# Performance work log

Measured on AMD Instinct MI355X. Metric: run time of the kernel, lower is better.

## Reference

```python
import math
import jax, jax.numpy as jnp
import numpy as np
from jax import lax

RADIUS = 3
KSIZE = 2 * RADIUS + 1  # 7
TOP_K = 8
SINKHORN_ITERS = 5


def _box_sum(x, h_axis, w_axis):
    # sum pooling with same padding over spatial axes
    wd = [1] * x.ndim
    wd[h_axis] = KSIZE
    wd[w_axis] = KSIZE
    pads = [(0, 0)] * x.ndim
    pads[h_axis] = (RADIUS, RADIUS)
    pads[w_axis] = (RADIUS, RADIUS)
    return lax.reduce_window(x, 0.0, lax.add, tuple(wd), (1,) * x.ndim, pads)


def geo_validate(src_pos, cand_pos, H, W):
    # src_pos [B,N,2], cand_pos [B,N,K,2] -> score [B,N,K]
    B, N, K, _ = cand_pos.shape
    src = src_pos.reshape(B, H, W, 1, 2)
    cand = cand_pos.reshape(B, H, W, K, 2)
    disp = cand - src  # [B,H,W,K,2]
    # count_include_pad=False -> divide by number of valid (in-bounds) taps
    cnt = _box_sum(jnp.ones((1, H, W, 1, 1), disp.dtype), 1, 2)
    mean = _box_sum(disp, 1, 2) / cnt
    mean_sq = _box_sum(disp * disp, 1, 2) / cnt
    var = jnp.clip(mean_sq - mean * mean, 0.0)
    total_var = var.sum(-1).reshape(B, N, K)
    return 1.0 / (1.0 + 100.0 * total_var)


def optimal_transport(scores, dustbin):
    B, M, N = scores.shape
    row = jnp.broadcast_to(dustbin, (B, M, 1))
    col = jnp.broadcast_to(dustbin, (B, 1, N))
    corner = jnp.zeros((B, 1, 1), scores.dtype)
    Z = jnp.concatenate([jnp.concatenate([scores, row], 2),
                         jnp.concatenate([col, corner], 2)], 1)  # [B,M+1,N+1]
    norm = -math.log(M + N)
    log_mu = jnp.full((M + 1,), norm, scores.dtype).at[M].set(math.log(N) + norm)
    log_nu = jnp.full((N + 1,), norm, scores.dtype).at[N].set(math.log(M) + norm)
    log_mu = jnp.broadcast_to(log_mu, (B, M + 1))
    log_nu = jnp.broadcast_to(log_nu, (B, N + 1))

    def body(_, uv):
        u, v = uv
        u = log_mu - jax.nn.logsumexp(Z + v[:, None, :], axis=2)
        v = log_nu - jax.nn.logsumexp(Z + u[:, :, None], axis=1)
        return (u, v)

    u0 = jnp.zeros((B, M + 1), scores.dtype)
    v0 = jnp.zeros((B, N + 1), scores.dtype)
    u, v = lax.fori_loop(0, SINKHORN_ITERS, body, (u0, v0))
    log_assign = Z + u[:, :, None] + v[:, None, :]
    return log_assign[:, :M, :N]


def solve_weighted_affine(src_pts, dst_pts, weights):
    # src/dst [B,N,2], weights [B,N,1] -> H_mat [B,3,3]
    B, N, _ = src_pts.shape
    w = weights[..., 0]
    w = w / jnp.clip(w.sum(1, keepdims=True), 1e-6)
    x, y = src_pts[..., 0], src_pts[..., 1]
    one = jnp.ones_like(x)
    zero = jnp.zeros_like(x)
    row_x = jnp.stack([x, y, one, zero, zero, zero], -1)   # [B,N,6]
    row_y = jnp.stack([zero, zero, zero, x, y, one], -1)
    A = jnp.concatenate([row_x, row_y], 1)                 # [B,2N,6]
    b = jnp.concatenate([dst_pts[..., 0], dst_pts[..., 1]], 1)[..., None]
    wd = jnp.concatenate([w, w], 1)[..., None]             # [B,2N,1]
    Aw = A * wd
    AtWA = jnp.einsum('bni,bnj->bij', Aw, A) + 1e-4 * jnp.eye(6, dtype=A.dtype)
    AtWb = jnp.einsum('bni,bnk->bik', Aw, b)
    p = jnp.linalg.solve(AtWA, AtWb)[..., 0]               # [B,6]
    a_, b_, c_, d_, e_, f_ = [p[:, i] for i in range(6)]
    z = jnp.zeros_like(a_)
    o = jnp.ones_like(a_)
    return jnp.stack([a_, b_, c_, d_, e_, f_, z, z, o], -1).reshape(B, 3, 3)


def matcher_forward(feat_A, feat_B, pos_A, pos_B, dustbin_score, geo_weight,
                    current_temp, H, W):
    B, N, C = feat_A.shape
    temp = current_temp[0]
    nA = feat_A / jnp.clip(jnp.linalg.norm(feat_A, axis=-1, keepdims=True), 1e-12)
    nB = feat_B / jnp.clip(jnp.linalg.norm(feat_B, axis=-1, keepdims=True), 1e-12)
    scores = jnp.einsum('bnc,bmc->bnm', nA, nB) / temp      # [B,N,N]
    log_assign = optimal_transport(scores, dustbin_score[0])
    ot_prob = jnp.exp(log_assign)
    topk_vals, topk_idx = lax.top_k(ot_prob, TOP_K)          # [B,N,K]
    bidx = jnp.arange(B)[:, None, None]
    topk_pos = pos_B[bidx, topk_idx]                         # [B,N,K,2]
    geo = geo_validate(pos_A, topk_pos, H, W)                # [B,N,K]
    gw = jnp.clip(geo_weight[0], 0.0, 2.0)
    combined = topk_vals + gw * geo
    soft = jax.nn.softmax(combined / temp, axis=-1)
    refined_warp = (topk_pos * soft[..., None]).sum(2)       # [B,N,2]
    conf = (soft * topk_vals).sum(-1, keepdims=True)         # [B,N,1]
    H_mat = solve_weighted_affine(pos_A, refined_warp, conf)
    return refined_warp, conf, H_mat


def setup_inputs() -> dict:
    key = jax.random.key(0)
    kA, kB, kP = jax.random.split(key, 3)
    B, H, W, C = 2, 64, 64, 128
    N = H * W
    feat_A = jax.random.normal(kA, (B, N, C), jnp.float32)
    feat_B = jax.random.normal(kB, (B, N, C), jnp.float32)
    # dense grid positions, normalized to [0,1]
    ys, xs = jnp.meshgrid(jnp.arange(H, dtype=jnp.float32),
                          jnp.arange(W, dtype=jnp.float32), indexing='ij')
    grid = jnp.stack([xs, ys], -1).reshape(1, N, 2) / float(max(H, W))
    pos_A = jnp.broadcast_to(grid, (B, N, 2))
    pos_B = pos_A + 0.01 * jax.random.normal(kP, (B, N, 2), jnp.float32)
    return {
        'feat_A': feat_A, 'feat_B': feat_B,
        'pos_A': pos_A, 'pos_B': pos_B,
        'dustbin_score': jnp.full((1,), -1.0, jnp.float32),
        'geo_weight': jnp.full((1,), 0.5, jnp.float32),
        'current_temp': jnp.full((1,), 0.1, jnp.float32),
        'H': H, 'W': W,
    }


def reference(feat_A, feat_B, pos_A, pos_B, dustbin_score, geo_weight,
              current_temp, H, W):
    return matcher_forward(feat_A, feat_B, pos_A, pos_B, dustbin_score,
                           geo_weight, current_temp, H, W)
```

## Files before the change

kernel.cpp:

```cpp
#include <hip/hip_runtime.h>
#include <math.h>

#define UVS 4104

#define OFF_ZU    33554432ul
#define OFF_WV    (OFF_ZU + 2*UVS)
#define OFF_RN    (OFF_WV + 2*UVS)
#define OFF_PARTS (OFF_RN + 16384)
#define OFF_TKV   (OFF_PARTS + 4194304)
#define OFF_TKP   (OFF_TKV + 65536)
#define OFF_DP    (OFF_TKP + 131072)
#define OFF_GEO   (OFF_DP + 131072)
#define OFF_SUM   (OFF_GEO + 65536)

#define EXPC    0.0001220703125f
#define HALFC   0.5f

#define PLANE   1048576

typedef __attribute__((ext_vector_type(8))) short bf16x8;
typedef __attribute__((ext_vector_type(4))) float f32x4;

static __device__ __forceinline__ unsigned f2bf(float x) {
    unsigned u = __float_as_uint(x);
    return (u + 0x7FFFu + ((u >> 16) & 1u)) >> 16;
}
static __device__ __forceinline__ float bf2f(unsigned h) { return __uint_as_float(h << 16); }

__global__ __launch_bounds__(256) void init_kernel(float* __restrict__ wv)
{
    int i = blockIdx.x * 256 + threadIdx.x;
    if (i < 2 * UVS) wv[i] = 1.0f;
}

__global__ __launch_bounds__(256) void norms_kernel(
    const float* __restrict__ fA, const float* __restrict__ fB, float* __restrict__ rn)
{
    int t = threadIdx.x;
    int rowg = blockIdx.x * 4 + (t >> 6);
    int lane = t & 63;
    const float* f = (rowg < 8192) ? fA : fB;
    int r = rowg & 8191;
    float x0 = f[(size_t)r * 128 + lane];
    float x1 = f[(size_t)r * 128 + 64 + lane];
    float s = x0 * x0 + x1 * x1;
    #pragma unroll
    for (int off = 32; off > 0; off >>= 1) s += __shfl_xor(s, off, 64);
    if (lane == 0) rn[rowg] = 1.f / fmaxf(sqrtf(s), 1e-12f);
}

__global__ __launch_bounds__(256) void pack_kernel(
    const float* __restrict__ fA, const float* __restrict__ fB, short* __restrict__ pk)
{
    int gt = blockIdx.x * 256 + threadIdx.x;
    int tensor = gt >> 17;
    int t = gt & 131071;
    int fr = t & 15;
    int kc = (t >> 4) & 15;
    int rb = (t >> 8) & 255;
    int b  = t >> 16;
    const float* src = tensor ? fB : fA;
    const float* p = src + ((size_t)(b * 4096 + rb * 16 + fr)) * 128 + kc * 8;
    float4 v0 = *(const float4*)p;
    float4 v1 = *(const float4*)(p + 4);
    float el[8] = {v0.x, v0.y, v0.z, v0.w, v1.x, v1.y, v1.z, v1.w};
    unsigned h[8], l[8];
    #pragma unroll
    for (int e = 0; e < 8; e++) { h[e] = f2bf(el[e]); l[e] = f2bf(el[e] - bf2f(h[e])); }
    uint4 hw = make_uint4(h[0] | (h[1] << 16), h[2] | (h[3] << 16),
                          h[4] | (h[5] << 16), h[6] | (h[7] << 16));
    uint4 lw = make_uint4(l[0] | (l[1] << 16), l[2] | (l[3] << 16),
                          l[4] | (l[5] << 16), l[6] | (l[7] << 16));
    size_t off = ((size_t)(b * 256 + rb)) * 2048 + kc * 128 + fr * 8;
    short* hi = pk + (size_t)tensor * 2 * PLANE;
    *(uint4*)(hi + off) = hw;
    *(uint4*)(hi + PLANE + off) = lw;
}

__global__ __launch_bounds__(256) void gemm_mfma(
    const short* __restrict__ pk, const float* __restrict__ rn,
    const float* __restrict__ temp, float* __restrict__ E0)
{
    __shared__ short Bs[16384];
    int b = blockIdx.z;
    int i0 = blockIdx.y * 64, j0 = blockIdx.x * 64;
    int t = threadIdx.x;
    int wave = t >> 6, lane = t & 63;
    int fr = lane & 15;
    int quad = lane >> 4;

    const short* gBhi = pk + 2 * (size_t)PLANE + ((size_t)(b * 256 + (j0 >> 4))) * 2048;
    const short* gBlo = gBhi + PLANE;
    #pragma unroll
    for (int c = 0; c < 4; c++) {
        int ch = c * 256 + t;
        *(uint4*)&Bs[ch * 8]        = *(const uint4*)(gBhi + ch * 8);
        *(uint4*)&Bs[8192 + ch * 8] = *(const uint4*)(gBlo + ch * 8);
    }

    const short* Abase_hi = pk + ((size_t)(b * 256 + (i0 >> 4) + wave)) * 2048;
    const short* Abase_lo = Abase_hi + PLANE;
    bf16x8 ah[4], al[4];
    #pragma unroll
    for (int s = 0; s < 4; s++) {
        ah[s] = *(const bf16x8*)(Abase_hi + s * 512 + lane * 8);
        al[s] = *(const bf16x8*)(Abase_lo + s * 512 + lane * 8);
    }
    __syncthreads();

    f32x4 acc[4] = {f32x4{0,0,0,0}, f32x4{0,0,0,0}, f32x4{0,0,0,0}, f32x4{0,0,0,0}};
    #pragma unroll
    for (int s = 0; s < 4; s++) {
        int lo = s * 512 + lane * 8;
        #pragma unroll
        for (int nb = 0; nb < 4; nb++) {
            bf16x8 bh = *(const bf16x8*)&Bs[nb * 2048 + lo];
            bf16x8 bl = *(const bf16x8*)&Bs[8192 + nb * 2048 + lo];
            acc[nb] = __builtin_amdgcn_mfma_f32_16x16x32_bf16(ah[s], bh, acc[nb], 0, 0, 0);
            acc[nb] = __builtin_amdgcn_mfma_f32_16x16x32_bf16(al[s], bh, acc[nb], 0, 0, 0);
            acc[nb] = __builtin_amdgcn_mfma_f32_16x16x32_bf16(ah[s], bl, acc[nb], 0, 0, 0);
        }
    }

    float invt = 1.f / temp[0];
    int m0 = i0 + wave * 16 + quad * 4;
    float ra[4];
    #pragma unroll
    for (int rr = 0; rr < 4; rr++) ra[rr] = rn[b * 4096 + m0 + rr] * invt;
    #pragma unroll
    for (int nb = 0; nb < 4; nb++) {
        int col = j0 + nb * 16 + fr;
        float rbv = rn[8192 + b * 4096 + col];
        #pragma unroll
        for (int rr = 0; rr < 4; rr++)
            E0[((size_t)(b * 4096 + m0 + rr)) * 4096 + col] = __expf(acc[nb][rr] * (ra[rr] * rbv));
    }
}

__global__ __launch_bounds__(64) void sink_fused(
    const float* __restrict__ E0, float* __restrict__ zu, const float* __restrict__ wv,
    const float* __restrict__ dbp, float* __restrict__ parts)
{
    int b = blockIdx.z;
    int lane = threadIdx.x;
    int ch = blockIdx.x;
    const float* wb = wv + b * UVS;
    float edb = __expf(dbp[0]);

    if (ch == 0) {
        float sv = 0.f;
        #pragma unroll
        for (int c = 0; c < 16; c++) {
            f32x4 w4 = *(const f32x4*)(wb + lane * 4 + c * 256);
            sv += (w4.x + w4.y) + (w4.z + w4.w);
        }
        #pragma unroll
        for (int off = 32; off > 0; off >>= 1) sv += __shfl_xor(sv, off, 64);
        if (lane == 0) zu[b * UVS + 4096] = HALFC / (edb * sv + wb[4096]);
    }

    float dtail = edb * wb[4096];
    f32x4 cacc[16];
    #pragma unroll
    for (int c = 0; c < 16; c++) cacc[c] = f32x4{0, 0, 0, 0};

    const float* Eb = E0 + ((size_t)b << 24);
    int base = lane * 4;

    for (int r = 0; r < 8; r++) {
        int row = ch * 8 + r;
        const float* Erow = Eb + ((size_t)row << 12);
        f32x4 x4[16];
        #pragma unroll
        for (int c = 0; c < 16; c++) x4[c] = *(const f32x4*)(Erow + base + c * 256);
        f32x4 rs4 = f32x4{0, 0, 0, 0};
        #pragma unroll
        for (int c = 0; c < 16; c++) {
            f32x4 w4 = *(const f32x4*)(wb + base + c * 256);
            rs4 += x4[c] * w4;
        }
        float rs = (rs4.x + rs4.y) + (rs4.z + rs4.w);
        #pragma unroll
        for (int off = 32; off > 0; off >>= 1) rs += __shfl_xor(rs, off, 64);
        float zi = EXPC / (rs + dtail);
        if (lane == 0) zu[b * UVS + row] = zi;
        #pragma unroll
        for (int c = 0; c < 16; c++) cacc[c] += x4[c] * zi;
    }

    float* pp = parts + ((size_t)(b * 512 + ch)) * 4096;
    #pragma unroll
    for (int c = 0; c < 16; c++) *(f32x4*)(pp + base + c * 256) = cacc[c];
}

__global__ __launch_bounds__(256) void sink_vB(
    const float* __restrict__ parts, const float* __restrict__ zu,
    float* __restrict__ wv, const float* __restrict__ dbp)
{
    int b = blockIdx.z;
    int t = threadIdx.x;
    float edb = __expf(dbp[0]);
    if (blockIdx.x < 16) {
        int j = blockIdx.x * 256 + t;
        float s = 0.f;
        #pragma unroll 16
        for (int ch = 0; ch < 512; ch++) s += parts[((size_t)(b * 512 + ch)) * 4096 + j];
        float total = s + edb * zu[b * UVS + 4096];
        wv[b * UVS + j] = EXPC / total;
    } else {
        __shared__ float red[256];
        float s = 0.f;
        for (int i = t; i < 4096; i += 256) s += zu[b * UVS + i];
        red[t] = s; __syncthreads();
        for (int off = 128; off > 0; off >>= 1) {
            if (t < off) red[t] += red[t + off];
            __syncthreads();
        }
        if (t == 0)
            wv[b * UVS + 4096] = HALFC / (edb * red[0] + zu[b * UVS + 4096]);
    }
}

#define FCMPSWAP(a, b) { float _mx = fmaxf(a, b), _mn = fminf(a, b); (a) = _mx; (b) = _mn; }
__global__ __launch_bounds__(256) void topk_kernel(
    const float* __restrict__ E0, const float* __restrict__ zu, const float* __restrict__ wv,
    const float* __restrict__ posA, const float* __restrict__ posB,
    float* __restrict__ tkv, float* __restrict__ tkp, float* __restrict__ dp)
{
    int wave = threadIdx.x >> 6;
    int lane = threadIdx.x & 63;
    int row = blockIdx.x * 4 + wave;
    int b = row >> 12; int i = row & 4095;
    const float* Erow = E0 + (size_t)row * 4096;
    const float* wb = wv + b * UVS;

    __shared__ unsigned long long cand[4][64];
    __shared__ int ccnt[4];
    if (lane == 0) ccnt[wave] = 0;

    f32x4 q[16];
    float s[8] = {0, 0, 0, 0, 0, 0, 0, 0};
    #pragma unroll
    for (int c = 0; c < 16; c++) {
        int j = c * 256 + lane * 4;
        f32x4 x = *(const f32x4*)(Erow + j);
        f32x4 w = *(const f32x4*)(wb + j);
        q[c] = x * w;
        float el[4] = {q[c].x, q[c].y, q[c].z, q[c].w};
        #pragma unroll
        for (int e = 0; e < 4; e++) {
            float xv = el[e];
            s[7] = __builtin_amdgcn_fmed3f(s[6], s[7], xv);
            s[6] = __builtin_amdgcn_fmed3f(s[5], s[6], xv);
            s[5] = __builtin_amdgcn_fmed3f(s[4], s[5], xv);
            s[4] = __builtin_amdgcn_fmed3f(s[3], s[4], xv);
            s[3] = __builtin_amdgcn_fmed3f(s[2], s[3], xv);
            s[2] = __builtin_amdgcn_fmed3f(s[1], s[2], xv);
            s[1] = __builtin_amdgcn_fmed3f(s[0], s[1], xv);
            s[0] = fmaxf(s[0], xv);
        }
    }

    #pragma unroll
    for (int st = 0; st < 6; st++) {
        int off = 1 << st;
        float o[8];
        #pragma unroll
        for (int r = 0; r < 8; r++) o[r] = __shfl_xor(s[r], off, 64);
        float m[8];
        #pragma unroll
        for (int r = 0; r < 8; r++) m[r] = fmaxf(s[r], o[7 - r]);
        FCMPSWAP(m[0], m[4]); FCMPSWAP(m[1], m[5]); FCMPSWAP(m[2], m[6]); FCMPSWAP(m[3], m[7]);
        FCMPSWAP(m[0], m[2]); FCMPSWAP(m[1], m[3]); FCMPSWAP(m[4], m[6]); FCMPSWAP(m[5], m[7]);
        FCMPSWAP(m[0], m[1]); FCMPSWAP(m[2], m[3]); FCMPSWAP(m[4], m[5]); FCMPSWAP(m[6], m[7]);
        #pragma unroll
        for (int r = 0; r < 8; r++) s[r] = m[r];
    }
    float t8 = s[7];

    __syncthreads();

    #pragma unroll
    for (int c = 0; c < 16; c++) {
        float el[4] = {q[c].x, q[c].y, q[c].z, q[c].w};
        #pragma unroll
        for (int e = 0; e < 4; e++) {
            if (el[e] >= t8) {
                int j = c * 256 + lane * 4 + e;
                unsigned long long key =
                    ((unsigned long long)__float_as_uint(el[e]) << 32) | (unsigned)(4095 - j);
                int slot = atomicAdd(&ccnt[wave], 1);
                if (slot < 64) cand[wave][slot] = key;
            }
        }
    }
    __syncthreads();

    int cnt = ccnt[wave]; if (cnt > 64) cnt = 64;
    if (lane < cnt) {
        unsigned long long my = cand[wave][lane];
        int rank = 0;
        for (int j2 = 0; j2 < cnt; j2++) rank += (cand[wave][j2] > my) ? 1 : 0;
        if (rank < 8) {
            int idx = 4095 - (int)(my & 0xFFFFFFFFu);
            float candv = __uint_as_float((unsigned)(my >> 32));
            float val = candv * zu[b * UVS + i];
            float px = posB[((size_t)(b * 4096 + idx)) * 2 + 0];
            float py = posB[((size_t)(b * 4096 + idx)) * 2 + 1];
            float ax = posA[((size_t)(b * 4096 + i)) * 2 + 0];
            float ay = posA[((size_t)(b * 4096 + i)) * 2 + 1];
            size_t base = ((size_t)(b * 4096 + i)) * 8 + rank;
            tkv[base] = val;
            tkp[base * 2 + 0] = px; tkp[base * 2 + 1] = py;
            dp[((size_t)((b * 8 + rank) * 2 + 0)) * 4096 + i] = px - ax;
            dp[((size_t)((b * 8 + rank) * 2 + 1)) * 4096 + i] = py - ay;
        }
    }
}

__global__ __launch_bounds__(256) void geo_kernel(
    const float* __restrict__ dp, float* __restrict__ geo)
{
    int tid = blockIdx.x * 256 + threadIdx.x;
    int n = tid & 4095; int bk = tid >> 12;
    int b = bk >> 3; int k = bk & 7;
    int h = n >> 6, w = n & 63;
    const float* dpx = dp + ((size_t)(bk * 2 + 0)) * 4096;
    const float* dpy = dp + ((size_t)(bk * 2 + 1)) * 4096;
    float sx = 0, sy = 0, sxx = 0, syy = 0, cnt = 0;
    #pragma unroll
    for (int dy = -3; dy <= 3; dy++) {
        int hh = h + dy; if ((unsigned)hh >= 64u) continue;
        #pragma unroll
        for (int dx = -3; dx <= 3; dx++) {
            int ww = w + dx; if ((unsigned)ww >= 64u) continue;
            int nn = (hh << 6) + ww;
            float vx = dpx[nn], vy = dpy[nn];
            sx += vx; sy += vy; sxx += vx * vx; syy += vy * vy; cnt += 1.f;
        }
    }
    float inv = 1.f / cnt;
    float mx = sx * inv, my = sy * inv;
    float varx = fmaxf(sxx * inv - mx * mx, 0.f);
    float vary = fmaxf(syy * inv - my * my, 0.f);
    geo[((size_t)(b * 4096 + n)) * 8 + k] = 1.f / (1.f + 100.f * (varx + vary));
}

__global__ __launch_bounds__(256) void refine_kernel(
    const float* __restrict__ tkv, const float* __restrict__ geo,
    const float* __restrict__ tkp, const float* __restrict__ gwp,
    const float* __restrict__ tpp, float* __restrict__ out)
{
    int tid = blockIdx.x * 256 + threadIdx.x;
    float gw = fminf(fmaxf(gwp[0], 0.f), 2.f);
    float invt = 1.f / tpp[0];
    size_t base = (size_t)tid * 8;
    float cb[8], vv[8];
    float mx = -INFINITY;
    #pragma unroll
    for (int k = 0; k < 8; k++) { vv[k] = tkv[base + k]; cb[k] = vv[k] + gw * geo[base + k]; mx = fmaxf(mx, cb[k]); }
    float e[8], se = 0;
    #pragma unroll
    for (int k = 0; k < 8; k++) { e[k] = __expf((cb[k] - mx) * invt); se += e[k]; }
    float wx = 0, wy = 0, cf = 0; float inv = 1.f / se;
    #pragma unroll
    for (int k = 0; k < 8; k++) {
        float s = e[k] * inv;
        wx += s * tkp[(base + k) * 2 + 0];
        wy += s * tkp[(base + k) * 2 + 1];
        cf += s * vv[k];
    }
    out[(size_t)tid * 2 + 0] = wx;
    out[(size_t)tid * 2 + 1] = wy;
    out[16384 + tid] = cf;
}

__global__ __launch_bounds__(256) void affine_reduce(
    const float* __restrict__ posA, const float* __restrict__ out, double* __restrict__ sums)
{
    int b = blockIdx.x; int t = threadIdx.x;
    double acc[12] = {0,0,0,0,0,0,0,0,0,0,0,0};
    for (int n = t; n < 4096; n += 256) {
        size_t idx = (size_t)b * 4096 + n;
        float x = posA[idx * 2], y = posA[idx * 2 + 1];
        float dx = out[idx * 2], dy = out[idx * 2 + 1];
        float c = out[16384 + idx];
        double cd = (double)c;
        double cx = cd * x, cy = cd * y;
        acc[0] += cx * x;  acc[1] += cx * y;  acc[2] += cy * y;
        acc[3] += cx;      acc[4] += cy;      acc[5] += cd;
        acc[6] += cx * dx; acc[7] += cy * dx; acc[8] += cd * dx;
        acc[9] += cx * dy; acc[10] += cy * dy; acc[11] += cd * dy;
    }
    __shared__ double red[256];
    for (int s = 0; s < 12; s++) {
        red[t] = acc[s]; __syncthreads();
        for (int off = 128; off > 0; off >>= 1) {
            if (t < off) red[t] += red[t + off];
            __syncthreads();
        }
        if (t == 0) sums[b * 12 + s] = red[0];
        __syncthreads();
    }
}

__global__ void affine_solve(const double* __restrict__ sums, float* __restrict__ out)
{
    int t = threadIdx.x;
    if (t >= 2) return;
    int b = t;
    const double* s = sums + b * 12;
    double den = s[5] > 1e-6 ? s[5] : 1e-6;
    double g00 = s[0] / den + 1e-4, g01 = s[1] / den, g02 = s[3] / den;
    double g11 = s[2] / den + 1e-4, g12 = s[4] / den;
    double g22 = s[5] / den + 1e-4;
    double bx0 = s[6] / den, bx1 = s[7] / den, bx2 = s[8] / den;
    double by0 = s[9] / den, by1 = s[10] / den, by2 = s[11] / den;
    double c00 = g11 * g22 - g12 * g12;
    double c01 = g02 * g12 - g01 * g22;
    double c02 = g01 * g12 - g02 * g11;
    double det = g00 * c00 + g01 * c01 + g02 * c02;
    double id = 1.0 / det;
    double i00 = c00 * id, i01 = c01 * id, i02 = c02 * id;
    double i11 = (g00 * g22 - g02 * g02) * id, i12 = (g01 * g02 - g00 * g12) * id;
    double i22 = (g00 * g11 - g01 * g01) * id;
    double a_ = i00 * bx0 + i01 * bx1 + i02 * bx2;
    double b_ = i01 * bx0 + i11 * bx1 + i12 * bx2;
    double c_ = i02 * bx0 + i12 * bx1 + i22 * bx2;
    double d_ = i00 * by0 + i01 * by1 + i02 * by2;
    double e_ = i01 * by0 + i11 * by1 + i12 * by2;
    double f_ = i02 * by0 + i12 * by1 + i22 * by2;
    float* o = out + 24576 + b * 9;
    o[0] = (float)a_; o[1] = (float)b_; o[2] = (float)c_;
    o[3] = (float)d_; o[4] = (float)e_; o[5] = (float)f_;
    o[6] = 0.f; o[7] = 0.f; o[8] = 1.f;
}

extern "C" void kernel_launch(void* const* d_in, const int* in_sizes, int n_in,
                              void* d_out, int out_size, void* d_ws, size_t ws_size,
                              hipStream_t stream) {
    const float* fA = (const float*)d_in[0];
    const float* fB = (const float*)d_in[1];
    const float* pA = (const float*)d_in[2];
    const float* pB = (const float*)d_in[3];
    const float* db = (const float*)d_in[4];
    const float* gw = (const float*)d_in[5];
    const float* tp = (const float*)d_in[6];

    float* ws    = (float*)d_ws;
    float* out   = (float*)d_out;
    float* E0    = ws;
    float* zu    = ws + OFF_ZU;
    float* wv    = ws + OFF_WV;
    float* rn    = ws + OFF_RN;
    float* parts = ws + OFF_PARTS;
    short* pk    = (short*)(ws + OFF_PARTS);
    float* tkv   = ws + OFF_TKV;
    float* tkp   = ws + OFF_TKP;
    float* dp    = ws + OFF_DP;
    float* geo   = ws + OFF_GEO;
    double* sums = (double*)(ws + OFF_SUM);

    init_kernel<<<33, 256, 0, stream>>>(wv);
    norms_kernel<<<4096, 256, 0, stream>>>(fA, fB, rn);
    pack_kernel<<<1024, 256, 0, stream>>>(fA, fB, pk);
    gemm_mfma<<<dim3(64, 64, 2), 256, 0, stream>>>(pk, rn, tp, E0);

    for (int it = 0; it < 5; it++) {
        sink_fused<<<dim3(512, 1, 2), 64, 0, stream>>>(E0, zu, wv, db, parts);
        sink_vB<<<dim3(17, 1, 2), 256, 0, stream>>>(parts, zu, wv, db);
    }

    topk_kernel<<<2048, 256, 0, stream>>>(E0, zu, wv, pA, pB, tkv, tkp, dp);
    geo_kernel<<<256, 256, 0, stream>>>(dp, geo);
    refine_kernel<<<32, 256, 0, stream>>>(tkv, geo, tkp, gw, tp, out);
    affine_reduce<<<2, 256, 0, stream>>>(pA, out, sums);
    affine_solve<<<1, 64, 0, stream>>>(sums, out);
}
```

Baseline: 395.4 us.

## Reduce Sinkhorn partials in shared memory and parallelize column reduction wider

The row-scaling kernel now uses 256-thread blocks of four waves, each wave handling 4 rows. The four per-wave column accumulators are summed in shared memory, which halves the number of partial-sum rows written to global memory (512 down to 256 per batch). The column-reduction kernel spreads each column's 256 partials over 4 thread groups across 64 blocks instead of 16, with a shared-memory final sum, so more of the GPU works on that serial reduction. The cost is 64KB of LDS per block, which limits occupancy, plus an extra barrier.

Measured after the change: 323.3 us. 1.22x faster.

```diff
diff --git a/kernel.cpp b/kernel.cpp
--- a/kernel.cpp
+++ b/kernel.cpp
@@ -7,7 +7,7 @@
 #define OFF_WV    (OFF_ZU + 2*UVS)
 #define OFF_RN    (OFF_WV + 2*UVS)
 #define OFF_PARTS (OFF_RN + 16384)
-#define OFF_TKV   (OFF_PARTS + 4194304)
+#define OFF_TKV   (OFF_PARTS + 2097152)
 #define OFF_TKP   (OFF_TKV + 65536)
 #define OFF_DP    (OFF_TKP + 131072)
 #define OFF_GEO   (OFF_DP + 131072)
@@ -137,17 +137,19 @@
     }
 }
 
-__global__ __launch_bounds__(64) void sink_fused(
+__global__ __launch_bounds__(256) void sink_fused(
     const float* __restrict__ E0, float* __restrict__ zu, const float* __restrict__ wv,
     const float* __restrict__ dbp, float* __restrict__ parts)
 {
     int b = blockIdx.z;
-    int lane = threadIdx.x;
-    int ch = blockIdx.x;
+    int t = threadIdx.x;
+    int wave = t >> 6, lane = t & 63;
+    int chb = blockIdx.x;
     const float* wb = wv + b * UVS;
     float edb = __expf(dbp[0]);
-
-    if (ch == 0) {
+    __shared__ float S[4][4096];
+
+    if (chb == 0 && wave == 0) {
         float sv = 0.f;
         #pragma unroll
         for (int c = 0; c < 16; c++) {
@@ -167,8 +169,8 @@
     const float* Eb = E0 + ((size_t)b << 24);
     int base = lane * 4;
 
-    for (int r = 0; r < 8; r++) {
-        int row = ch * 8 + r;
+    for (int r = 0; r < 4; r++) {
+        int row = chb * 16 + wave * 4 + r;
         const float* Erow = Eb + ((size_t)row << 12);
         f32x4 x4[16];
         #pragma unroll
@@ -188,9 +190,15 @@
         for (int c = 0; c < 16; c++) cacc[c] += x4[c] * zi;
     }
 
-    float* pp = parts + ((size_t)(b * 512 + ch)) * 4096;
-    #pragma unroll
-    for (int c = 0; c < 16; c++) *(f32x4*)(pp + base + c * 256) = cacc[c];
+    #pragma unroll
+    for (int c = 0; c < 16; c++) *(f32x4*)&S[wave][base + c * 256] = cacc[c];
+    __syncthreads();
+    float* pp = parts + ((size_t)(b * 256 + chb)) * 4096;
+    #pragma unroll
+    for (int k = 0; k < 16; k++) {
+        int col = t + k * 256;
+        pp[col] = (S[0][col] + S[1][col]) + (S[2][col] + S[3][col]);
+    }
 }
 
 __global__ __launch_bounds__(256) void sink_vB(
@@ -200,24 +208,32 @@
     int b = blockIdx.z;
     int t = threadIdx.x;
     float edb = __expf(dbp[0]);
-    if (blockIdx.x < 16) {
-        int j = blockIdx.x * 256 + t;
+    if (blockIdx.x < 64) {
+        int col = blockIdx.x * 64 + (t & 63);
+        int grp = t >> 6;
         float s = 0.f;
-        #pragma unroll 16
-        for (int ch = 0; ch < 512; ch++) s += parts[((size_t)(b * 512 + ch)) * 4096 + j];
-        float total = s + edb * zu[b * UVS + 4096];
-        wv[b * UVS + j] = EXPC / total;
+        #pragma unroll 8
+        for (int ch = grp * 64; ch < grp * 64 + 64; ch++)
+            s += parts[((size_t)(b * 256 + ch)) * 4096 + col];
+        __shared__ float red[4][64];
+        red[grp][t & 63] = s;
+        __syncthreads();
+        if (grp == 0) {
+            float tot = (red[0][t] + red[1][t]) + (red[2][t] + red[3][t]);
+            tot += edb * zu[b * UVS + 4096];
+            wv[b * UVS + col] = EXPC / tot;
+        }
     } else {
-        __shared__ float red[256];
+        __shared__ float red2[256];
         float s = 0.f;
         for (int i = t; i < 4096; i += 256) s += zu[b * UVS + i];
-        red[t] = s; __syncthreads();
+        red2[t] = s; __syncthreads();
         for (int off = 128; off > 0; off >>= 1) {
-            if (t < off) red[t] += red[t + off];
+            if (t < off) red2[t] += red2[t + off];
             __syncthreads();
         }
         if (t == 0)
-            wv[b * UVS + 4096] = HALFC / (edb * red[0] + zu[b * UVS + 4096]);
+            wv[b * UVS + 4096] = HALFC / (edb * red2[0] + zu[b * UVS + 4096]);
     }
 }
 
@@ -467,8 +483,8 @@
     gemm_mfma<<<dim3(64, 64, 2), 256, 0, stream>>>(pk, rn, tp, E0);
 
     for (int it = 0; it < 5; it++) {
-        sink_fused<<<dim3(512, 1, 2), 64, 0, stream>>>(E0, zu, wv, db, parts);
-        sink_vB<<<dim3(17, 1, 2), 256, 0, stream>>>(parts, zu, wv, db);
+        sink_fused<<<dim3(256, 1, 2), 256, 0, stream>>>(E0, zu, wv, db, parts);
+        sink_vB<<<dim3(65, 1, 2), 256, 0, stream>>>(parts, zu, wv, db);
     }
 
     topk_kernel<<<2048, 256, 0, stream>>>(E0, zu, wv, pA, pB, tkv, tkp, dp);
```
